# Kernel tuning notes

Hardware: AMD Instinct MI355X
Metric: run time of the kernel (lower is better)

## Reference

```python
import jax, jax.numpy as jnp
import numpy as np
from jax import lax

STRIDES = [4, 8, 16, 32, 64]
SIZES = [32.0, 64.0, 128.0, 256.0, 512.0]
RATIOS = [0.5, 1.0, 2.0]
IMG_H = IMG_W = 1024.0
NMS_T = 0.7
PRE = 1000      # PRE_NMS_TOPK_TEST
POST = 1000     # POST_NMS_TOPK_TEST
MIN_SIZE = 0.0
N = 2
FEAT = [(256, 256), (128, 128), (64, 64), (32, 32), (16, 16)]
SCALE_CLAMP = float(np.log(1000.0 / 16.0))


def make_anchors(H, W, stride, size):
    # detectron2 DefaultAnchorGenerator: area=size^2, w=sqrt(area/r), h=w*r; grid offsets = stride*arange
    r = np.array(RATIOS)
    ws = np.sqrt(size * size / r)
    hs = ws * r
    base = np.stack([-ws / 2, -hs / 2, ws / 2, hs / 2], axis=1)  # [A,4]
    sx = np.arange(W) * stride
    sy = np.arange(H) * stride
    yy, xx = np.meshgrid(sy, sx, indexing='ij')
    shifts = np.stack([xx, yy, xx, yy], axis=-1).reshape(-1, 1, 4)  # [H*W,1,4]
    return jnp.asarray((shifts + base[None]).reshape(-1, 4), jnp.float32)  # [H*W*A,4]


def conv2d(x, w, b, pad):
    y = lax.conv_general_dilated(x, w, (1, 1), [(pad, pad), (pad, pad)],
                                 dimension_numbers=('NCHW', 'OIHW', 'NCHW'))
    return y + b[None, :, None, None]


def apply_deltas(deltas, anchors):
    # Box2BoxTransform.apply_deltas with weights (1,1,1,1)
    w = anchors[..., 2] - anchors[..., 0]
    h = anchors[..., 3] - anchors[..., 1]
    cx = anchors[..., 0] + 0.5 * w
    cy = anchors[..., 1] + 0.5 * h
    dx, dy, dw, dh = deltas[..., 0], deltas[..., 1], deltas[..., 2], deltas[..., 3]
    dw = jnp.minimum(dw, SCALE_CLAMP)
    dh = jnp.minimum(dh, SCALE_CLAMP)
    pcx = dx * w + cx
    pcy = dy * h + cy
    pw = jnp.exp(dw) * w
    ph = jnp.exp(dh) * h
    return jnp.stack([pcx - 0.5 * pw, pcy - 0.5 * ph, pcx + 0.5 * pw, pcy + 0.5 * ph], axis=-1)


def pairwise_iou(b):
    area = (b[:, 2] - b[:, 0]) * (b[:, 3] - b[:, 1])
    lt = jnp.maximum(b[:, None, :2], b[None, :, :2])
    rb = jnp.minimum(b[:, None, 2:], b[None, :, 2:])
    wh = jnp.clip(rb - lt, 0.0)
    inter = wh[..., 0] * wh[..., 1]
    return inter / jnp.maximum(area[:, None] + area[None, :] - inter, 1e-9)


def nms_keep(boxes, valid):
    # boxes already sorted by score desc; sequential greedy NMS keep mask
    K = boxes.shape[0]
    M = pairwise_iou(boxes)
    idx = jnp.arange(K)

    def body(i, keep):
        sup = (M[i] > NMS_T) & (idx > i) & keep[i]
        return keep & (~sup)

    return lax.fori_loop(0, K, body, valid)


def rpn_forward(feats, conv_w, conv_b, obj_w, obj_b, delta_w, delta_b):
    all_boxes, all_scores = [], []
    lim = jnp.array([IMG_W, IMG_H, IMG_W, IMG_H], jnp.float32)
    for x, (H, W), stride, size in zip(feats, FEAT, STRIDES, SIZES):
        t = jax.nn.relu(conv2d(x, conv_w, conv_b, 1))
        logits = conv2d(t, obj_w, obj_b, 0)      # [N,A,H,W]
        deltas = conv2d(t, delta_w, delta_b, 0)  # [N,4A,H,W]
        A = logits.shape[1]
        logits = logits.transpose(0, 2, 3, 1).reshape(N, -1)                       # [N,H*W*A]
        deltas = deltas.reshape(N, A, 4, H, W).transpose(0, 3, 4, 1, 2).reshape(N, -1, 4)
        anchors = make_anchors(H, W, stride, size)
        props = apply_deltas(deltas, anchors[None])                                # [N,H*W*A,4]
        k = min(PRE, props.shape[1])
        scores, idx = lax.top_k(logits, k)                                         # [N,k]
        boxes = jnp.take_along_axis(props, idx[..., None], axis=1)                 # [N,k,4]
        boxes = jnp.clip(boxes, 0.0, lim)                                          # clip to image
        valid = ((boxes[..., 2] - boxes[..., 0]) > MIN_SIZE) & ((boxes[..., 3] - boxes[..., 1]) > MIN_SIZE)
        keep = lax.stop_gradient(jax.vmap(nms_keep)(boxes, valid))                 # NMS is no_grad in torch
        all_boxes.append(boxes)
        all_scores.append(jnp.where(keep, scores, -1e9))
    boxes = jnp.concatenate(all_boxes, axis=1)
    scores = jnp.concatenate(all_scores, axis=1)
    fs, fi = lax.top_k(scores, POST)                                               # final sort-by-score
    fb = jnp.take_along_axis(boxes, fi[..., None], axis=1)
    return fb, fs


def setup_inputs() -> dict:
    key = jax.random.key(0)
    ks = jax.random.split(key, 8)
    d = {}
    for i, (name, (H, W)) in enumerate(zip(['p2', 'p3', 'p4', 'p5', 'p6'], FEAT)):
        d[name] = jax.random.normal(ks[i], (N, 256, H, W), jnp.float32)
    d['conv_w'] = jax.random.normal(ks[5], (256, 256, 3, 3), jnp.float32) * 0.01
    d['conv_b'] = jnp.zeros((256,), jnp.float32)
    d['obj_w'] = jax.random.normal(ks[6], (3, 256, 1, 1), jnp.float32) * 0.01
    d['obj_b'] = jnp.zeros((3,), jnp.float32)
    d['delta_w'] = jax.random.normal(ks[7], (12, 256, 1, 1), jnp.float32) * 0.01
    d['delta_b'] = jnp.zeros((12,), jnp.float32)
    return d


def reference(p2, p3, p4, p5, p6, conv_w, conv_b, obj_w, obj_b, delta_w, delta_b):
    return rpn_forward([p2, p3, p4, p5, p6], conv_w, conv_b, obj_w, obj_b, delta_w, delta_b)
```

## Files before the change

kernel.cpp:

```cpp
#include <hip/hip_runtime.h>
#include <stdint.h>

#define DEVI __device__ __forceinline__

#define S_TOT 261888
#define NIMG  2
#define SCLD  4.135166556742356

__constant__ int    c_S[5]    = {196608, 49152, 12288, 3072, 768};
__constant__ int    c_loff[5] = {0, 196608, 245760, 258048, 261120};
__constant__ int    c_K[5]    = {1000, 1000, 1000, 1000, 768};
__constant__ int    c_Wl[5]   = {256, 128, 64, 32, 16};
__constant__ int    c_str[5]  = {4, 8, 16, 32, 64};
__constant__ double c_sz[5]   = {32.0, 64.0, 128.0, 256.0, 512.0};
__constant__ double c_rat[3]  = {0.5, 1.0, 2.0};
__constant__ int    c_boff[6] = {0, 512, 640, 672, 680, 682};
__constant__ int    c_Hl[5]   = {256, 128, 64, 32, 16};

DEVI unsigned key_of(float f) {
  unsigned u = __float_as_uint(f);
  return (u & 0x80000000u) ? ~u : (u | 0x80000000u);
}
DEVI float key_dec(unsigned k) {
  unsigned u = (k & 0x80000000u) ? (k & 0x7fffffffu) : ~k;
  return __uint_as_float(u);
}

__global__ void transpose_w(const float* __restrict__ w, float* __restrict__ wT3) {
  int k  = blockIdx.x;
  int co = threadIdx.x;
  int ci = k / 9, j = k - ci * 9;
  int chunk = ci >> 3, cc = ci & 7;
  int g = co >> 5, i = co & 31;
  wT3[(size_t)chunk * 18432 + cc * 2304 + g * 288 + j * 32 + i] = w[co * 2304 + k];
}

__global__ __launch_bounds__(512, 4) void conv_fused(
    const float* __restrict__ x0, const float* __restrict__ x1,
    const float* __restrict__ x2, const float* __restrict__ x3,
    const float* __restrict__ x4,
    const float* __restrict__ wT3,
    const float* __restrict__ cb, const float* __restrict__ ow,
    const float* __restrict__ ob, const float* __restrict__ dwt,
    const float* __restrict__ db, float* __restrict__ logits,
    float* __restrict__ deltas)
{
  __shared__ float lds[19872];
  float* const wlds = lds + 1440;
  const int tid = threadIdx.x;
  const int n = blockIdx.y;
  const int b = blockIdx.x;
  int l = 0;
#pragma unroll
  for (int q = 1; q < 5; ++q) if (b >= c_boff[q]) l = q;
  const int t = b - c_boff[l];
  const int H = c_Hl[l], W = H;
  const int tilesx = 16 >> l;
  const int tx = t & (tilesx - 1), ty = t >> (4 - l);
  const int px0 = tx << 4, py0 = ty << 3;
  const int loff = c_loff[l];
  const float* xin = (l == 0) ? x0 : (l == 1) ? x1 : (l == 2) ? x2 : (l == 3) ? x3 : x4;
  xin += (size_t)n * 256 * H * W;

  const int lane = tid & 63, wv = tid >> 6;
  const int px = lane & 15, p = lane >> 4;

  float a0[32], a1[32];
#pragma unroll
  for (int i = 0; i < 32; ++i) { a0[i] = 0.f; a1[i] = 0.f; }

  for (int ch = 0; ch < 32; ++ch) {
    const int ci0 = ch << 3;
    __syncthreads();
    for (int tt = tid; tt < 1440; tt += 512) {
      int ci = tt / 180, rem = tt - ci * 180;
      int ry = rem / 18, rx = rem - ry * 18;
      int gy = py0 + ry - 1, gx = px0 + rx - 1;
      float v = 0.f;
      if (gy >= 0 && gy < H && gx >= 0 && gx < W)
        v = xin[((size_t)(ci0 + ci) * H + gy) * W + gx];
      lds[tt] = v;
    }
    {
      const float4* wg = (const float4*)(wT3 + (size_t)ch * 18432);
      float4* wl = (float4*)wlds;
      for (int tt = tid; tt < 4608; tt += 512) wl[tt] = wg[tt];
    }
    __syncthreads();
#pragma unroll 1
    for (int cc = 0; cc < 8; ++cc) {
      const float* wr = wlds + cc * 2304 + wv * 288;
      const int pb = cc * 180 + p * 18 + px;
#pragma unroll 1
      for (int ky = 0; ky < 3; ++ky) {
        const int rb = pb + ky * 18;
        const float q00 = lds[rb + 0],  q01 = lds[rb + 1],  q02 = lds[rb + 2];
        const float q10 = lds[rb + 72], q11 = lds[rb + 73], q12 = lds[rb + 74];
        const float* wk = wr + ky * 96;
#pragma unroll
        for (int kx = 0; kx < 3; ++kx) {
          const float pv0 = (kx == 0) ? q00 : (kx == 1) ? q01 : q02;
          const float pv1 = (kx == 0) ? q10 : (kx == 1) ? q11 : q12;
          const float* wt = wk + kx * 32;
#pragma unroll
          for (int iq = 0; iq < 8; ++iq) {
            const float4 wq = *(const float4*)(wt + (iq << 2));
            a0[iq * 4 + 0] = fmaf(wq.x, pv0, a0[iq * 4 + 0]);
            a0[iq * 4 + 1] = fmaf(wq.y, pv0, a0[iq * 4 + 1]);
            a0[iq * 4 + 2] = fmaf(wq.z, pv0, a0[iq * 4 + 2]);
            a0[iq * 4 + 3] = fmaf(wq.w, pv0, a0[iq * 4 + 3]);
            a1[iq * 4 + 0] = fmaf(wq.x, pv1, a1[iq * 4 + 0]);
            a1[iq * 4 + 1] = fmaf(wq.y, pv1, a1[iq * 4 + 1]);
            a1[iq * 4 + 2] = fmaf(wq.z, pv1, a1[iq * 4 + 2]);
            a1[iq * 4 + 3] = fmaf(wq.w, pv1, a1[iq * 4 + 3]);
          }
        }
      }
    }
  }

  const int co0 = __builtin_amdgcn_readfirstlane(wv << 5);
#pragma unroll
  for (int h = 0; h < 2; ++h) {
    float part[15];
#pragma unroll
    for (int f = 0; f < 15; ++f) part[f] = 0.f;
#pragma unroll
    for (int i = 0; i < 32; ++i) {
      float v = (h ? a1[i] : a0[i]) + cb[co0 + i];
      float tv = fmaxf(v, 0.f);
#pragma unroll
      for (int f = 0; f < 3; ++f)  part[f]     = fmaf(tv, ow[f * 256 + co0 + i],  part[f]);
#pragma unroll
      for (int f = 0; f < 12; ++f) part[3 + f] = fmaf(tv, dwt[f * 256 + co0 + i], part[3 + f]);
    }
    __syncthreads();
#pragma unroll
    for (int f = 0; f < 15; ++f) lds[wv * 960 + f * 64 + lane] = part[f];
    __syncthreads();
    for (int tt = tid; tt < 960; tt += 512) {
      float s = 0.f;
#pragma unroll
      for (int w2 = 0; w2 < 8; ++w2) s += lds[w2 * 960 + tt];
      int f = tt >> 6, pp = tt & 63;
      int gx = px0 + (pp & 15), gy = py0 + (pp >> 4) + 4 * h;
      int cell = gy * W + gx;
      if (f < 3) {
        logits[(size_t)n * S_TOT + loff + cell * 3 + f] = s + ob[f];
      } else {
        int chn = f - 3, a = chn >> 2, c = chn & 3;
        deltas[(((size_t)n * S_TOT + loff + cell * 3 + a) << 2) + c] = s + db[chn];
      }
    }
  }
}

__global__ __launch_bounds__(1024) void topk_kernel(
    const float* __restrict__ logits, const float* __restrict__ deltas,
    float* __restrict__ selscore, float* __restrict__ selbox,
    unsigned* __restrict__ selvalid)
{
  const int tid = threadIdx.x;
  const int nl = blockIdx.x, n = nl / 5, l = nl % 5;
  const int Sl = c_S[l], loff = c_loff[l], Kl = c_K[l], Wl = c_Wl[l], strl = c_str[l];
  const float* sc = logits + (size_t)n * S_TOT + loff;

  __shared__ unsigned hist[256];
  __shared__ unsigned sh_prefix, sh_need, s_base, s_cb;
  __shared__ unsigned waveTot[16], waveOff[16];
  __shared__ unsigned long long sortbuf[1024];

  unsigned prefix = 0, need = (unsigned)Kl;
  for (int p = 0; p < 4; ++p) {
    for (int i = tid; i < 256; i += 1024) hist[i] = 0;
    __syncthreads();
    const int shift = 24 - p * 8;
    for (int i = tid; i < Sl; i += 1024) {
      unsigned k = key_of(sc[i]);
      if (p == 0 || (k >> (shift + 8)) == prefix)
        atomicAdd(&hist[(k >> shift) & 255u], 1u);
    }
    __syncthreads();
    if (tid == 0) {
      unsigned cum = 0;
      for (int b = 255; b >= 0; --b) {
        unsigned c = hist[b];
        if (cum + c >= need) { sh_prefix = (prefix << 8) | (unsigned)b; sh_need = need - cum; break; }
        cum += c;
      }
    }
    __syncthreads();
    prefix = sh_prefix; need = sh_need;
    __syncthreads();
  }
  const unsigned Tkey = prefix;

  if (tid == 0) s_base = 0;
  __syncthreads();
  for (int pass = 0; pass < 2; ++pass) {
    for (int st = 0; st < Sl; st += 1024) {
      const int i = st + tid;
      bool flag = false; unsigned k = 0;
      if (i < Sl) {
        k = key_of(sc[i]);
        flag = (pass == 0) ? (k > Tkey) : (k == Tkey);
      }
      unsigned long long m = __ballot(flag);
      const int lane = tid & 63, w = tid >> 6;
      unsigned mypre = (unsigned)__popcll(m & ((1ull << lane) - 1ull));
      if (lane == 0) waveTot[w] = (unsigned)__popcll(m);
      __syncthreads();
      if (tid == 0) {
        unsigned ss = 0;
        for (int q = 0; q < 16; ++q) { waveOff[q] = ss; ss += waveTot[q]; }
        s_cb = s_base; s_base += ss;
      }
      __syncthreads();
      if (flag) {
        unsigned pos = s_cb + waveOff[w] + mypre;
        if (pos < (unsigned)Kl)
          sortbuf[pos] = (((unsigned long long)k) << 32) |
                         (unsigned long long)(0xFFFFFFFFu - (unsigned)i);
      }
      __syncthreads();
    }
  }
  if (tid >= Kl) sortbuf[tid] = (unsigned long long)(0xFFFFFFFFu - (unsigned)tid);
  __syncthreads();

  for (int k2 = 2; k2 <= 1024; k2 <<= 1) {
    for (int j = k2 >> 1; j > 0; j >>= 1) {
      const int i = tid, ixj = i ^ j;
      if (ixj > i) {
        unsigned long long a = sortbuf[i], b = sortbuf[ixj];
        const bool desc = (i & k2) == 0;
        if (desc ? (a < b) : (a > b)) { sortbuf[i] = b; sortbuf[ixj] = a; }
      }
      __syncthreads();
    }
  }

  const int r = tid;
  const int o = nl * 1024 + r;
  if (r < Kl) {
    unsigned long long v = sortbuf[r];
    unsigned k = (unsigned)(v >> 32);
    unsigned ai = 0xFFFFFFFFu - (unsigned)(v & 0xFFFFFFFFull);
    float score = key_dec(k);
    int cell = (int)(ai / 3u), a = (int)(ai % 3u);
    int xg = cell % Wl, yg = cell / Wl;
    double rr = c_rat[a], sz = c_sz[l];
    double wsd = sqrt(sz * sz / rr);
    double hw = 0.5 * wsd, hh = 0.5 * wsd * rr;
    double xs = (double)(xg * strl), ys = (double)(yg * strl);
    float a0 = (float)(xs - hw), a1 = (float)(ys - hh);
    float a2 = (float)(xs + hw), a3 = (float)(ys + hh);
    const float* dp = deltas + (((size_t)n * S_TOT + loff + ai) << 2);
    float dx = dp[0], dy = dp[1], dw_ = dp[2], dh_ = dp[3];
    float aw = a2 - a0, ah = a3 - a1;
    float cx = a0 + 0.5f * aw, cy = a1 + 0.5f * ah;
    dw_ = fminf(dw_, (float)SCLD); dh_ = fminf(dh_, (float)SCLD);
    float pcx = dx * aw + cx, pcy = dy * ah + cy;
    float pw = expf(dw_) * aw, ph = expf(dh_) * ah;
    float b0 = fminf(fmaxf(pcx - 0.5f * pw, 0.f), 1024.f);
    float b1 = fminf(fmaxf(pcy - 0.5f * ph, 0.f), 1024.f);
    float b2 = fminf(fmaxf(pcx + 0.5f * pw, 0.f), 1024.f);
    float b3 = fminf(fmaxf(pcy + 0.5f * ph, 0.f), 1024.f);
    unsigned valid = ((b2 - b0) > 0.f && (b3 - b1) > 0.f) ? 1u : 0u;
    selscore[o] = score;
    selbox[o * 4 + 0] = b0; selbox[o * 4 + 1] = b1;
    selbox[o * 4 + 2] = b2; selbox[o * 4 + 3] = b3;
    selvalid[o] = valid;
  } else {
    selscore[o] = -1e9f;
    selbox[o * 4 + 0] = 0.f; selbox[o * 4 + 1] = 0.f;
    selbox[o * 4 + 2] = 0.f; selbox[o * 4 + 3] = 0.f;
    selvalid[o] = 0u;
  }
}

__global__ __launch_bounds__(256) void nms_sup(
    const float* __restrict__ selbox, unsigned long long* __restrict__ sup)
{
  int gid = blockIdx.x * 256 + threadIdx.x;
  int w = gid & 15, i = (gid >> 4) & 1023, nl = gid >> 14;
  if (nl >= 10) return;
  int l = nl % 5, Kl = c_K[l];
  unsigned long long bits = 0;
  if (i < Kl) {
    const float* bi = selbox + (size_t)(nl * 1024 + i) * 4;
    float x0 = bi[0], y0 = bi[1], x1 = bi[2], y1 = bi[3];
    float ar = (x1 - x0) * (y1 - y0);
    int jlo = w * 64; if (jlo < i + 1) jlo = i + 1;
    int jhi = w * 64 + 64; if (jhi > Kl) jhi = Kl;
    for (int j = jlo; j < jhi; ++j) {
      const float* bj = selbox + (size_t)(nl * 1024 + j) * 4;
      float u0 = fmaxf(x0, bj[0]), v0 = fmaxf(y0, bj[1]);
      float u1 = fminf(x1, bj[2]), v1 = fminf(y1, bj[3]);
      float iw = fmaxf(u1 - u0, 0.f), ih = fmaxf(v1 - v0, 0.f);
      float inter = iw * ih;
      float aj = (bj[2] - bj[0]) * (bj[3] - bj[1]);
      float iou = inter / fmaxf(ar + aj - inter, 1e-9f);
      if (iou > 0.7f) bits |= 1ull << (j - w * 64);
    }
  }
  sup[(size_t)(nl * 1024 + i) * 16 + w] = bits;
}

__global__ __launch_bounds__(64) void nms_reduce(
    const unsigned* __restrict__ selvalid, const unsigned long long* __restrict__ sup,
    const float* __restrict__ selscore, float* __restrict__ scnms)
{
  const int nl = blockIdx.x, tid = threadIdx.x;
  const int l = nl % 5, Kl = c_K[l];
  unsigned long long keep = 0;
  if (tid < 16) {
    for (int t = 0; t < 64; ++t) {
      int r = tid * 64 + t;
      if (r < Kl && selvalid[nl * 1024 + r]) keep |= 1ull << t;
    }
  }
  const unsigned long long* srow = sup + (size_t)nl * 1024 * 16;
  unsigned long long rowA = (tid < 16) ? srow[(size_t)0 * 16 + tid] : 0;
  unsigned long long rowB = (tid < 16 && Kl > 1) ? srow[(size_t)1 * 16 + tid] : 0;
  for (int i = 0; i < Kl; i += 2) {
    unsigned long long kw = __shfl(keep, i >> 6);
    unsigned long long cur = rowA;
    rowA = (tid < 16 && i + 2 < Kl) ? srow[(size_t)(i + 2) * 16 + tid] : 0;
    if (((kw >> (i & 63)) & 1ull) && tid < 16) keep &= ~cur;
    kw = __shfl(keep, (i + 1) >> 6);
    cur = rowB;
    rowB = (tid < 16 && i + 3 < Kl) ? srow[(size_t)(i + 3) * 16 + tid] : 0;
    if (((kw >> ((i + 1) & 63)) & 1ull) && tid < 16) keep &= ~cur;
  }
  for (int r = tid; r < 1024; r += 64) {
    unsigned long long wv = __shfl(keep, r >> 6);
    bool kp = (r < Kl) && ((wv >> (r & 63)) & 1ull);
    scnms[nl * 1024 + r] = kp ? selscore[nl * 1024 + r] : -1e9f;
  }
}

DEVI float cand_score(const float* scnms, int n, int g) {
  int l = g / 1000;
  int r = g - l * 1000;
  return scnms[((n * 5 + l) << 10) + r];
}

__global__ __launch_bounds__(1024) void final_topk(
    const float* __restrict__ scnms, const float* __restrict__ selbox,
    float* __restrict__ out)
{
  const int tid = threadIdx.x;
  const int n = blockIdx.x;
  const int S = 4768;

  __shared__ unsigned hist[256];
  __shared__ unsigned sh_prefix, sh_need, s_base, s_cb;
  __shared__ unsigned waveTot[16], waveOff[16];
  __shared__ unsigned long long sortbuf[1024];

  unsigned prefix = 0, need = 1000;
  for (int p = 0; p < 4; ++p) {
    for (int i = tid; i < 256; i += 1024) hist[i] = 0;
    __syncthreads();
    const int shift = 24 - p * 8;
    for (int i = tid; i < S; i += 1024) {
      unsigned k = key_of(cand_score(scnms, n, i));
      if (p == 0 || (k >> (shift + 8)) == prefix)
        atomicAdd(&hist[(k >> shift) & 255u], 1u);
    }
    __syncthreads();
    if (tid == 0) {
      unsigned cum = 0;
      for (int b = 255; b >= 0; --b) {
        unsigned c = hist[b];
        if (cum + c >= need) { sh_prefix = (prefix << 8) | (unsigned)b; sh_need = need - cum; break; }
        cum += c;
      }
    }
    __syncthreads();
    prefix = sh_prefix; need = sh_need;
    __syncthreads();
  }
  const unsigned Tkey = prefix;

  if (tid == 0) s_base = 0;
  __syncthreads();
  for (int pass = 0; pass < 2; ++pass) {
    for (int st = 0; st < S; st += 1024) {
      const int i = st + tid;
      bool flag = false; unsigned k = 0;
      if (i < S) {
        k = key_of(cand_score(scnms, n, i));
        flag = (pass == 0) ? (k > Tkey) : (k == Tkey);
      }
      unsigned long long m = __ballot(flag);
      const int lane = tid & 63, w = tid >> 6;
      unsigned mypre = (unsigned)__popcll(m & ((1ull << lane) - 1ull));
      if (lane == 0) waveTot[w] = (unsigned)__popcll(m);
      __syncthreads();
      if (tid == 0) {
        unsigned ss = 0;
        for (int q = 0; q < 16; ++q) { waveOff[q] = ss; ss += waveTot[q]; }
        s_cb = s_base; s_base += ss;
      }
      __syncthreads();
      if (flag) {
        unsigned pos = s_cb + waveOff[w] + mypre;
        if (pos < 1000u)
          sortbuf[pos] = (((unsigned long long)k) << 32) |
                         (unsigned long long)(0xFFFFFFFFu - (unsigned)i);
      }
      __syncthreads();
    }
  }
  if (tid >= 1000) sortbuf[tid] = (unsigned long long)(0xFFFFFFFFu - (unsigned)tid);
  __syncthreads();

  for (int k2 = 2; k2 <= 1024; k2 <<= 1) {
    for (int j = k2 >> 1; j > 0; j >>= 1) {
      const int i = tid, ixj = i ^ j;
      if (ixj > i) {
        unsigned long long a = sortbuf[i], b = sortbuf[ixj];
        const bool desc = (i & k2) == 0;
        if (desc ? (a < b) : (a > b)) { sortbuf[i] = b; sortbuf[ixj] = a; }
      }
      __syncthreads();
    }
  }

  if (tid < 1000) {
    unsigned long long v = sortbuf[tid];
    unsigned k = (unsigned)(v >> 32);
    int g = (int)(0xFFFFFFFFu - (unsigned)(v & 0xFFFFFFFFull));
    int l = g / 1000, r = g - l * 1000;
    const float* b = selbox + ((size_t)((n * 5 + l) * 1024 + r)) * 4;
    size_t ob_ = ((size_t)n * 1000 + tid) * 4;
    out[ob_ + 0] = b[0]; out[ob_ + 1] = b[1];
    out[ob_ + 2] = b[2]; out[ob_ + 3] = b[3];
    out[8000 + n * 1000 + tid] = key_dec(k);
  }
}

extern "C" void kernel_launch(void* const* d_in, const int* in_sizes, int n_in,
                              void* d_out, int out_size, void* d_ws, size_t ws_size,
                              hipStream_t stream)
{
  const float* feats[5];
  for (int i = 0; i < 5; ++i) feats[i] = (const float*)d_in[i];
  const float* conv_w  = (const float*)d_in[5];
  const float* conv_b  = (const float*)d_in[6];
  const float* obj_w   = (const float*)d_in[7];
  const float* obj_b   = (const float*)d_in[8];
  const float* delta_w = (const float*)d_in[9];
  const float* delta_b = (const float*)d_in[10];

  char* wsp = (char*)d_ws;
  float* wT3      = (float*)wsp;  wsp += (size_t)2304 * 256 * 4;
  float* logits   = (float*)wsp;  wsp += (size_t)NIMG * S_TOT * 4;
  float* deltas   = (float*)wsp;  wsp += (size_t)NIMG * S_TOT * 16;
  float* selscore = (float*)wsp;  wsp += (size_t)10 * 1024 * 4;
  float* selbox   = (float*)wsp;  wsp += (size_t)10 * 1024 * 16;
  unsigned* selvalid = (unsigned*)wsp; wsp += (size_t)10 * 1024 * 4;
  float* scnms    = (float*)wsp;  wsp += (size_t)10 * 1024 * 4;
  unsigned long long* sup = (unsigned long long*)wsp;
  wsp += (size_t)10 * 1024 * 16 * 8;

  transpose_w<<<dim3(2304), dim3(256), 0, stream>>>(conv_w, wT3);

  conv_fused<<<dim3(682, NIMG), dim3(512), 0, stream>>>(
      feats[0], feats[1], feats[2], feats[3], feats[4],
      wT3, conv_b, obj_w, obj_b, delta_w, delta_b, logits, deltas);

  topk_kernel<<<dim3(10), dim3(1024), 0, stream>>>(logits, deltas,
                                                   selscore, selbox, selvalid);
  nms_sup<<<dim3(640), dim3(256), 0, stream>>>(selbox, sup);
  nms_reduce<<<dim3(10), dim3(64), 0, stream>>>(selvalid, sup, selscore, scnms);
  final_topk<<<dim3(NIMG), dim3(1024), 0, stream>>>(scnms, selbox, (float*)d_out);
}
```

Before: 3.695 ms.

## Enlarge conv tile to 16x16 pixels with 1024-thread blocks and 64-accumulator register tiles

Measured after the change: 3.370 ms. -8.8%, faster.

```diff
diff --git a/kernel.cpp b/kernel.cpp
--- a/kernel.cpp
+++ b/kernel.cpp
@@ -14,7 +14,7 @@
 __constant__ int    c_str[5]  = {4, 8, 16, 32, 64};
 __constant__ double c_sz[5]   = {32.0, 64.0, 128.0, 256.0, 512.0};
 __constant__ double c_rat[3]  = {0.5, 1.0, 2.0};
-__constant__ int    c_boff[6] = {0, 512, 640, 672, 680, 682};
+__constant__ int    c_boff[6] = {0, 256, 320, 336, 340, 341};
 __constant__ int    c_Hl[5]   = {256, 128, 64, 32, 16};
 
 DEVI unsigned key_of(float f) {
@@ -26,27 +26,27 @@
   return __uint_as_float(u);
 }
 
-__global__ void transpose_w(const float* __restrict__ w, float* __restrict__ wT3) {
+__global__ void transpose_w(const float* __restrict__ w, float* __restrict__ wT4) {
   int k  = blockIdx.x;
   int co = threadIdx.x;
   int ci = k / 9, j = k - ci * 9;
   int chunk = ci >> 3, cc = ci & 7;
-  int g = co >> 5, i = co & 31;
-  wT3[(size_t)chunk * 18432 + cc * 2304 + g * 288 + j * 32 + i] = w[co * 2304 + k];
-}
-
-__global__ __launch_bounds__(512, 4) void conv_fused(
+  int g = co >> 4, i = co & 15;
+  wT4[(size_t)chunk * 18432 + cc * 2304 + g * 144 + j * 16 + i] = w[co * 2304 + k];
+}
+
+__global__ __launch_bounds__(1024, 4) void conv_fused(
     const float* __restrict__ x0, const float* __restrict__ x1,
     const float* __restrict__ x2, const float* __restrict__ x3,
     const float* __restrict__ x4,
-    const float* __restrict__ wT3,
+    const float* __restrict__ wT4,
     const float* __restrict__ cb, const float* __restrict__ ow,
     const float* __restrict__ ob, const float* __restrict__ dwt,
     const float* __restrict__ db, float* __restrict__ logits,
     float* __restrict__ deltas)
 {
-  __shared__ float lds[19872];
-  float* const wlds = lds + 1440;
+  __shared__ float lds[21024];
+  float* const wlds = lds + 2592;
   const int tid = threadIdx.x;
   const int n = blockIdx.y;
   const int b = blockIdx.x;
@@ -57,7 +57,7 @@
   const int H = c_Hl[l], W = H;
   const int tilesx = 16 >> l;
   const int tx = t & (tilesx - 1), ty = t >> (4 - l);
-  const int px0 = tx << 4, py0 = ty << 3;
+  const int px0 = tx << 4, py0 = ty << 4;
   const int loff = c_loff[l];
   const float* xin = (l == 0) ? x0 : (l == 1) ? x1 : (l == 2) ? x2 : (l == 3) ? x3 : x4;
   xin += (size_t)n * 256 * H * W;
@@ -65,15 +65,15 @@
   const int lane = tid & 63, wv = tid >> 6;
   const int px = lane & 15, p = lane >> 4;
 
-  float a0[32], a1[32];
-#pragma unroll
-  for (int i = 0; i < 32; ++i) { a0[i] = 0.f; a1[i] = 0.f; }
+  float acc[64];
+#pragma unroll
+  for (int i = 0; i < 64; ++i) acc[i] = 0.f;
 
   for (int ch = 0; ch < 32; ++ch) {
     const int ci0 = ch << 3;
     __syncthreads();
-    for (int tt = tid; tt < 1440; tt += 512) {
-      int ci = tt / 180, rem = tt - ci * 180;
+    for (int tt = tid; tt < 2592; tt += 1024) {
+      int ci = tt / 324, rem = tt - ci * 324;
       int ry = rem / 18, rx = rem - ry * 18;
       int gy = py0 + ry - 1, gx = px0 + rx - 1;
       float v = 0.f;
@@ -82,53 +82,81 @@
       lds[tt] = v;
     }
     {
-      const float4* wg = (const float4*)(wT3 + (size_t)ch * 18432);
+      const float4* wg = (const float4*)(wT4 + (size_t)ch * 18432);
       float4* wl = (float4*)wlds;
-      for (int tt = tid; tt < 4608; tt += 512) wl[tt] = wg[tt];
+      for (int tt = tid; tt < 4608; tt += 1024) wl[tt] = wg[tt];
     }
     __syncthreads();
 #pragma unroll 1
     for (int cc = 0; cc < 8; ++cc) {
-      const float* wr = wlds + cc * 2304 + wv * 288;
-      const int pb = cc * 180 + p * 18 + px;
+      const float* wr = wlds + cc * 2304 + wv * 144;
+      const int pb = cc * 324 + p * 18 + px;
 #pragma unroll 1
       for (int ky = 0; ky < 3; ++ky) {
         const int rb = pb + ky * 18;
-        const float q00 = lds[rb + 0],  q01 = lds[rb + 1],  q02 = lds[rb + 2];
-        const float q10 = lds[rb + 72], q11 = lds[rb + 73], q12 = lds[rb + 74];
-        const float* wk = wr + ky * 96;
+        float q0[3], q1[3], q2[3], q3[3];
+#pragma unroll
+        for (int c = 0; c < 3; ++c) {
+          q0[c] = lds[rb + c];
+          q1[c] = lds[rb + 72 + c];
+          q2[c] = lds[rb + 144 + c];
+          q3[c] = lds[rb + 216 + c];
+        }
+        const float* wk = wr + ky * 48;
 #pragma unroll
         for (int kx = 0; kx < 3; ++kx) {
-          const float pv0 = (kx == 0) ? q00 : (kx == 1) ? q01 : q02;
-          const float pv1 = (kx == 0) ? q10 : (kx == 1) ? q11 : q12;
-          const float* wt = wk + kx * 32;
-#pragma unroll
-          for (int iq = 0; iq < 8; ++iq) {
-            const float4 wq = *(const float4*)(wt + (iq << 2));
-            a0[iq * 4 + 0] = fmaf(wq.x, pv0, a0[iq * 4 + 0]);
-            a0[iq * 4 + 1] = fmaf(wq.y, pv0, a0[iq * 4 + 1]);
-            a0[iq * 4 + 2] = fmaf(wq.z, pv0, a0[iq * 4 + 2]);
-            a0[iq * 4 + 3] = fmaf(wq.w, pv0, a0[iq * 4 + 3]);
-            a1[iq * 4 + 0] = fmaf(wq.x, pv1, a1[iq * 4 + 0]);
-            a1[iq * 4 + 1] = fmaf(wq.y, pv1, a1[iq * 4 + 1]);
-            a1[iq * 4 + 2] = fmaf(wq.z, pv1, a1[iq * 4 + 2]);
-            a1[iq * 4 + 3] = fmaf(wq.w, pv1, a1[iq * 4 + 3]);
-          }
+          const float* wt = wk + kx * 16;
+          const float4 wa = *(const float4*)(wt + 0);
+          const float4 wb = *(const float4*)(wt + 4);
+          const float4 wc = *(const float4*)(wt + 8);
+          const float4 wd = *(const float4*)(wt + 12);
+          const float v0 = q0[kx], v1 = q1[kx], v2 = q2[kx], v3 = q3[kx];
+          acc[ 0] = fmaf(wa.x, v0, acc[ 0]); acc[ 1] = fmaf(wa.y, v0, acc[ 1]);
+          acc[ 2] = fmaf(wa.z, v0, acc[ 2]); acc[ 3] = fmaf(wa.w, v0, acc[ 3]);
+          acc[ 4] = fmaf(wb.x, v0, acc[ 4]); acc[ 5] = fmaf(wb.y, v0, acc[ 5]);
+          acc[ 6] = fmaf(wb.z, v0, acc[ 6]); acc[ 7] = fmaf(wb.w, v0, acc[ 7]);
+          acc[ 8] = fmaf(wc.x, v0, acc[ 8]); acc[ 9] = fmaf(wc.y, v0, acc[ 9]);
+          acc[10] = fmaf(wc.z, v0, acc[10]); acc[11] = fmaf(wc.w, v0, acc[11]);
+          acc[12] = fmaf(wd.x, v0, acc[12]); acc[13] = fmaf(wd.y, v0, acc[13]);
+          acc[14] = fmaf(wd.z, v0, acc[14]); acc[15] = fmaf(wd.w, v0, acc[15]);
+          acc[16] = fmaf(wa.x, v1, acc[16]); acc[17] = fmaf(wa.y, v1, acc[17]);
+          acc[18] = fmaf(wa.z, v1, acc[18]); acc[19] = fmaf(wa.w, v1, acc[19]);
+          acc[20] = fmaf(wb.x, v1, acc[20]); acc[21] = fmaf(wb.y, v1, acc[21]);
+          acc[22] = fmaf(wb.z, v1, acc[22]); acc[23] = fmaf(wb.w, v1, acc[23]);
+          acc[24] = fmaf(wc.x, v1, acc[24]); acc[25] = fmaf(wc.y, v1, acc[25]);
+          acc[26] = fmaf(wc.z, v1, acc[26]); acc[27] = fmaf(wc.w, v1, acc[27]);
+          acc[28] = fmaf(wd.x, v1, acc[28]); acc[29] = fmaf(wd.y, v1, acc[29]);
+          acc[30] = fmaf(wd.z, v1, acc[30]); acc[31] = fmaf(wd.w, v1, acc[31]);
+          acc[32] = fmaf(wa.x, v2, acc[32]); acc[33] = fmaf(wa.y, v2, acc[33]);
+          acc[34] = fmaf(wa.z, v2, acc[34]); acc[35] = fmaf(wa.w, v2, acc[35]);
+          acc[36] = fmaf(wb.x, v2, acc[36]); acc[37] = fmaf(wb.y, v2, acc[37]);
+          acc[38] = fmaf(wb.z, v2, acc[38]); acc[39] = fmaf(wb.w, v2, acc[39]);
+          acc[40] = fmaf(wc.x, v2, acc[40]); acc[41] = fmaf(wc.y, v2, acc[41]);
+          acc[42] = fmaf(wc.z, v2, acc[42]); acc[43] = fmaf(wc.w, v2, acc[43]);
+          acc[44] = fmaf(wd.x, v2, acc[44]); acc[45] = fmaf(wd.y, v2, acc[45]);
+          acc[46] = fmaf(wd.z, v2, acc[46]); acc[47] = fmaf(wd.w, v2, acc[47]);
+          acc[48] = fmaf(wa.x, v3, acc[48]); acc[49] = fmaf(wa.y, v3, acc[49]);
+          acc[50] = fmaf(wa.z, v3, acc[50]); acc[51] = fmaf(wa.w, v3, acc[51]);
+          acc[52] = fmaf(wb.x, v3, acc[52]); acc[53] = fmaf(wb.y, v3, acc[53]);
+          acc[54] = fmaf(wb.z, v3, acc[54]); acc[55] = fmaf(wb.w, v3, acc[55]);
+          acc[56] = fmaf(wc.x, v3, acc[56]); acc[57] = fmaf(wc.y, v3, acc[57]);
+          acc[58] = fmaf(wc.z, v3, acc[58]); acc[59] = fmaf(wc.w, v3, acc[59]);
+          acc[60] = fmaf(wd.x, v3, acc[60]); acc[61] = fmaf(wd.y, v3, acc[61]);
+          acc[62] = fmaf(wd.z, v3, acc[62]); acc[63] = fmaf(wd.w, v3, acc[63]);
         }
       }
     }
   }
 
-  const int co0 = __builtin_amdgcn_readfirstlane(wv << 5);
-#pragma unroll
-  for (int h = 0; h < 2; ++h) {
+  const int co0 = __builtin_amdgcn_readfirstlane(wv << 4);
+#pragma unroll
+  for (int h = 0; h < 4; ++h) {
     float part[15];
 #pragma unroll
     for (int f = 0; f < 15; ++f) part[f] = 0.f;
 #pragma unroll
-    for (int i = 0; i < 32; ++i) {
-      float v = (h ? a1[i] : a0[i]) + cb[co0 + i];
-      float tv = fmaxf(v, 0.f);
+    for (int i = 0; i < 16; ++i) {
+      float tv = fmaxf(acc[h * 16 + i] + cb[co0 + i], 0.f);
 #pragma unroll
       for (int f = 0; f < 3; ++f)  part[f]     = fmaf(tv, ow[f * 256 + co0 + i],  part[f]);
 #pragma unroll
@@ -138,10 +166,10 @@
 #pragma unroll
     for (int f = 0; f < 15; ++f) lds[wv * 960 + f * 64 + lane] = part[f];
     __syncthreads();
-    for (int tt = tid; tt < 960; tt += 512) {
+    for (int tt = tid; tt < 960; tt += 1024) {
       float s = 0.f;
 #pragma unroll
-      for (int w2 = 0; w2 < 8; ++w2) s += lds[w2 * 960 + tt];
+      for (int w2 = 0; w2 < 16; ++w2) s += lds[w2 * 960 + tt];
       int f = tt >> 6, pp = tt & 63;
       int gx = px0 + (pp & 15), gy = py0 + (pp >> 4) + 4 * h;
       int cell = gy * W + gx;
@@ -456,7 +484,7 @@
   const float* delta_b = (const float*)d_in[10];
 
   char* wsp = (char*)d_ws;
-  float* wT3      = (float*)wsp;  wsp += (size_t)2304 * 256 * 4;
+  float* wT4      = (float*)wsp;  wsp += (size_t)2304 * 256 * 4;
   float* logits   = (float*)wsp;  wsp += (size_t)NIMG * S_TOT * 4;
   float* deltas   = (float*)wsp;  wsp += (size_t)NIMG * S_TOT * 16;
   float* selscore = (float*)wsp;  wsp += (size_t)10 * 1024 * 4;
@@ -466,11 +494,11 @@
   unsigned long long* sup = (unsigned long long*)wsp;
   wsp += (size_t)10 * 1024 * 16 * 8;
 
-  transpose_w<<<dim3(2304), dim3(256), 0, stream>>>(conv_w, wT3);
-
-  conv_fused<<<dim3(682, NIMG), dim3(512), 0, stream>>>(
+  transpose_w<<<dim3(2304), dim3(256), 0, stream>>>(conv_w, wT4);
+
+  conv_fused<<<dim3(341, NIMG), dim3(1024), 0, stream>>>(
       feats[0], feats[1], feats[2], feats[3], feats[4],
-      wT3, conv_b, obj_w, obj_b, delta_w, delta_b, logits, deltas);
+      wT4, conv_b, obj_w, obj_b, delta_w, delta_b, logits, deltas);
 
   topk_kernel<<<dim3(10), dim3(1024), 0, stream>>>(logits, deltas,
                                                    selscore, selbox, selvalid);
```
